# Kernel optimization log

Measured on AMD Instinct MI355X. Metric: run time of the kernel, lower is better.

## Reference

```python
import jax, jax.numpy as jnp
import numpy as np

B, D, U = 4096, 256, 512


def setup_inputs() -> dict:
    key = jax.random.key(0)
    k = jax.random.split(key, 7)
    return {
        "x": jax.random.normal(k[0], (B, D), jnp.float32),
        "t": jax.random.uniform(k[1], (B, 1), jnp.float32),           # elapsed-time input
        "h0": jax.random.normal(k[2], (B, U), jnp.float32),
        "c0": jax.random.normal(k[3], (B, U), jnp.float32),
        "kernel": jax.random.normal(k[4], (D, 5 * U), jnp.float32) / np.sqrt(D).astype(np.float32),
        "recurrent_kernel": jax.random.normal(k[5], (U, 3 * U), jnp.float32) / np.sqrt(U).astype(np.float32),
        "kernel_time": jax.random.normal(k[6], (1, 3 * U), jnp.float32) * 0.1,
    }


def reference(x, t, h0, c0, kernel, recurrent_kernel, kernel_time):
    sig = jax.nn.sigmoid
    # Fused input projection: one GEMM instead of 5 (same math, kernel cols are
    # ordered [i, c, o, t1, t2] exactly as the original slices self.kernel).
    x_i, x_c, x_o, x_t1, x_t2 = jnp.split(x @ kernel, 5, axis=1)          # each (B, U)
    # Fused recurrent projection: cols ordered [i, c, o].
    r_i, r_c, r_o = jnp.split(h0 @ recurrent_kernel, 3, axis=1)           # each (B, U)
    # Time projections: cols ordered [t1, t2, o].
    kt1, kt2, kto = jnp.split(t @ kernel_time, 3, axis=1)                 # each (B, U)

    i = sig(x_i + r_i)
    t_1 = sig(x_t1 + sig(kt1))
    # tf.where(t_1 > -1e-5, -1e-5, t_1): sigmoid output is always > -1e-5,
    # so this clamps to the constant -1e-5; keep the where for faithfulness.
    NEG_EPS = jnp.float32(-1e-5)
    t_1_constraint = jnp.where(t_1 > NEG_EPS, jnp.full_like(t_1, NEG_EPS), t_1)
    t_2 = sig(x_t2 + sig(kt2))
    c_tilde = jnp.tanh(x_c + r_c)
    c_m_ = (1.0 - i * t_1) * c0 + i * c_tilde * t_1_constraint
    c_m = (1.0 - i) * c0 + i * c_tilde * t_2
    o = sig(x_o + r_o + kto)
    h = jnp.tanh(c_m_) * o
    # original returns (h, [h, c_m]); h appears twice, so return (h, c_m)
    return (h, c_m)
```

## Files before the change

kernel.cpp:

```cpp
#include <hip/hip_runtime.h>


typedef __attribute__((ext_vector_type(8))) short short8_t;
typedef __attribute__((ext_vector_type(4))) float f32x4_t;
typedef unsigned int u32;

#define B_N 4096
#define D_K 256
#define U_N 512

__device__ __forceinline__ unsigned short f2bf(float f) {
    unsigned int x = __float_as_uint(f);
    unsigned int r = x + 0x7fffu + ((x >> 16) & 1u);
    return (unsigned short)(r >> 16);
}

__device__ __forceinline__ float sigf(float z) {
    return 1.0f / (1.0f + __expf(-z));
}

__device__ __forceinline__ void gl16(const unsigned short* g, unsigned short* l) {
    __builtin_amdgcn_global_load_lds(
        (const __attribute__((address_space(1))) u32*)g,
        (__attribute__((address_space(3))) u32*)l, 16, 0, 0);
}

#define SWZ(r, kc) ((((r) * 8) + ((kc) ^ ((r) & 7))) * 8)

__global__ __launch_bounds__(256) void prep(
    const float* __restrict__ x, const float* __restrict__ h0,
    const float* __restrict__ kern, const float* __restrict__ rk,
    unsigned short* __restrict__ xs, unsigned short* __restrict__ hs,
    unsigned short* __restrict__ ksw, unsigned short* __restrict__ rsw)
{
    const int c = blockIdx.x * 256 + threadIdx.x;
    if (c < 131072) {
        const int t = c >> 10, q = c & 1023;
        const int row = q >> 3, kc = q & 7;
        const int rb = t >> 2, kb = t & 3;
        const float* s = x + (size_t)(rb * 128 + row) * D_K + kb * 64 + kc * 8;
        short8_t o;
#pragma unroll
        for (int j = 0; j < 8; ++j) o[j] = (short)f2bf(s[j]);
        *reinterpret_cast<short8_t*>(xs + (size_t)t * 8192 + SWZ(row, kc)) = o;
    } else if (c < 393216) {
        const int c2 = c - 131072;
        const int t = c2 >> 10, q = c2 & 1023;
        const int row = q >> 3, kc = q & 7;
        const int rb = t >> 3, kb = t & 7;
        const float* s = h0 + (size_t)(rb * 128 + row) * U_N + kb * 64 + kc * 8;
        short8_t o;
#pragma unroll
        for (int j = 0; j < 8; ++j) o[j] = (short)f2bf(s[j]);
        *reinterpret_cast<short8_t*>(hs + (size_t)t * 8192 + SWZ(row, kc)) = o;
    } else if (c < 475136) {
        const int c2 = c - 393216;
        const int t = c2 / 1280, q = c2 - t * 1280;
        const int kc = q / 160, r = q - kc * 160;
        const int nb = t >> 2, kb = t & 3;
        const int col = (r >> 5) * U_N + nb * 32 + (r & 31);
        short8_t o;
#pragma unroll
        for (int j = 0; j < 8; ++j)
            o[j] = (short)f2bf(kern[(size_t)(kb * 64 + kc * 8 + j) * 2560 + col]);
        *reinterpret_cast<short8_t*>(ksw + (size_t)t * 10240 + SWZ(r, kc)) = o;
    } else {
        const int c2 = c - 475136;
        const int t = c2 / 768, q = c2 - t * 768;
        const int kc = q / 96, r = q - kc * 96;
        const int nb = t >> 3, kb = t & 7;
        const int col = (r >> 5) * U_N + nb * 32 + (r & 31);
        short8_t o;
#pragma unroll
        for (int j = 0; j < 8; ++j)
            o[j] = (short)f2bf(rk[(size_t)(kb * 64 + kc * 8 + j) * 1536 + col]);
        *reinterpret_cast<short8_t*>(rsw + (size_t)t * 6144 + SWZ(r, kc)) = o;
    }
}

__global__ __launch_bounds__(256, 2) void tlstm_main(
    const unsigned short* __restrict__ xs,
    const unsigned short* __restrict__ hs,
    const unsigned short* __restrict__ ksw,
    const unsigned short* __restrict__ rsw,
    const float* __restrict__ tvec,
    const float* __restrict__ c0,
    const float* __restrict__ ktime,
    float* __restrict__ out)
{
    __shared__ __align__(16) unsigned short lds[2][18432];

    const int tid = threadIdx.x;
    const int wave = tid >> 6;
    const int lane = tid & 63;
    const int lr = lane & 15;
    const int lq = lane >> 4;
    const int nb = blockIdx.x;
    const int rb = blockIdx.y;

    f32x4_t acc[8][2][2];
#pragma unroll
    for (int m = 0; m < 8; ++m)
#pragma unroll
        for (int p = 0; p < 2; ++p)
#pragma unroll
            for (int n = 0; n < 2; ++n)
                acc[m][p][n] = (f32x4_t){0.f, 0.f, 0.f, 0.f};

    auto stage = [&](int s, int buf) {
        unsigned short* ab = &lds[buf][0];
        unsigned short* bb = &lds[buf][8192];
        if (s < 4) {
            const unsigned short* at = xs + (size_t)(rb * 4 + s) * 8192;
#pragma unroll
            for (int j = 0; j < 4; ++j)
                gl16(at + (j * 256 + tid) * 8, ab + (j * 256 + wave * 64) * 8);
            const unsigned short* bt = ksw + (size_t)(nb * 4 + s) * 10240;
#pragma unroll
            for (int j = 0; j < 5; ++j)
                gl16(bt + (j * 256 + tid) * 8, bb + (j * 256 + wave * 64) * 8);
        } else {
            const unsigned short* at = hs + (size_t)(rb * 8 + (s - 4)) * 8192;
#pragma unroll
            for (int j = 0; j < 4; ++j)
                gl16(at + (j * 256 + tid) * 8, ab + (j * 256 + wave * 64) * 8);
            const unsigned short* bt = rsw + (size_t)(nb * 8 + (s - 4)) * 6144;
#pragma unroll
            for (int j = 0; j < 3; ++j)
                gl16(bt + (j * 256 + tid) * 8, bb + (j * 256 + wave * 64) * 8);
        }
    };

    auto compute1 = [&](int buf) {
        const unsigned short* ab = &lds[buf][0];
        const unsigned short* bb = &lds[buf][8192];
#pragma unroll
        for (int ks = 0; ks < 2; ++ks) {
            const int kc = ks * 4 + lq;
            const int r0 = wave * 32 + lr;
            short8_t a0 = *reinterpret_cast<const short8_t*>(ab + SWZ(r0, kc));
            short8_t a1 = *reinterpret_cast<const short8_t*>(ab + SWZ(r0 + 16, kc));
#pragma unroll
            for (int m = 0; m < 5; ++m)
#pragma unroll
                for (int n = 0; n < 2; ++n) {
                    const int r = m * 32 + n * 16 + lr;
                    short8_t b = *reinterpret_cast<const short8_t*>(bb + SWZ(r, kc));
                    acc[m][0][n] = __builtin_amdgcn_mfma_f32_16x16x32_bf16(a0, b, acc[m][0][n], 0, 0, 0);
                    acc[m][1][n] = __builtin_amdgcn_mfma_f32_16x16x32_bf16(a1, b, acc[m][1][n], 0, 0, 0);
                }
        }
    };

    auto compute2 = [&](int buf) {
        const unsigned short* ab = &lds[buf][0];
        const unsigned short* bb = &lds[buf][8192];
#pragma unroll
        for (int ks = 0; ks < 2; ++ks) {
            const int kc = ks * 4 + lq;
            const int r0 = wave * 32 + lr;
            short8_t a0 = *reinterpret_cast<const short8_t*>(ab + SWZ(r0, kc));
            short8_t a1 = *reinterpret_cast<const short8_t*>(ab + SWZ(r0 + 16, kc));
#pragma unroll
            for (int m = 0; m < 3; ++m)
#pragma unroll
                for (int n = 0; n < 2; ++n) {
                    const int r = m * 32 + n * 16 + lr;
                    short8_t b = *reinterpret_cast<const short8_t*>(bb + SWZ(r, kc));
                    acc[5 + m][0][n] = __builtin_amdgcn_mfma_f32_16x16x32_bf16(a0, b, acc[5 + m][0][n], 0, 0, 0);
                    acc[5 + m][1][n] = __builtin_amdgcn_mfma_f32_16x16x32_bf16(a1, b, acc[5 + m][1][n], 0, 0, 0);
                }
        }
    };

    int cur = 0;
    stage(0, 0);
    __syncthreads();
#pragma unroll 1
    for (int s = 0; s < 12; ++s) {
        if (s < 11) stage(s + 1, cur ^ 1);
        if (s < 4) compute1(cur); else compute2(cur);
        __syncthreads();
        cur ^= 1;
    }

    const float NEG_EPS = -1e-5f;
#pragma unroll
    for (int n = 0; n < 2; ++n) {
        const int u = nb * 32 + n * 16 + lr;
        const float kt1 = ktime[u];
        const float kt2 = ktime[U_N + u];
        const float kto = ktime[2 * U_N + u];
#pragma unroll
        for (int p = 0; p < 2; ++p)
#pragma unroll
            for (int i2 = 0; i2 < 4; ++i2) {
                const int b = rb * 128 + wave * 32 + p * 16 + lq * 4 + i2;
                const float tb = tvec[b];
                const float c0v = c0[(size_t)b * U_N + u];
                const float x_i  = acc[0][p][n][i2];
                const float x_c  = acc[1][p][n][i2];
                const float x_o  = acc[2][p][n][i2];
                const float x_t1 = acc[3][p][n][i2];
                const float x_t2 = acc[4][p][n][i2];
                const float r_i  = acc[5][p][n][i2];
                const float r_c  = acc[6][p][n][i2];
                const float r_o  = acc[7][p][n][i2];

                const float ig  = sigf(x_i + r_i);
                const float t1v = sigf(x_t1 + sigf(tb * kt1));
                const float t1c = (t1v > NEG_EPS) ? NEG_EPS : t1v;
                const float t2v = sigf(x_t2 + sigf(tb * kt2));
                const float ct  = tanhf(x_c + r_c);
                const float cm_ = (1.f - ig * t1v) * c0v + ig * ct * t1c;
                const float cm  = (1.f - ig) * c0v + ig * ct * t2v;
                const float og  = sigf(x_o + r_o + tb * kto);

                out[(size_t)b * U_N + u] = tanhf(cm_) * og;
                out[(size_t)B_N * U_N + (size_t)b * U_N + u] = cm;
            }
    }
}

extern "C" void kernel_launch(void* const* d_in, const int* in_sizes, int n_in,
                              void* d_out, int out_size, void* d_ws, size_t ws_size,
                              hipStream_t stream) {
    const float* x     = (const float*)d_in[0];
    const float* t     = (const float*)d_in[1];
    const float* h0    = (const float*)d_in[2];
    const float* c0    = (const float*)d_in[3];
    const float* kern  = (const float*)d_in[4];
    const float* rk    = (const float*)d_in[5];
    const float* ktime = (const float*)d_in[6];
    float* out = (float*)d_out;

    unsigned short* xs  = (unsigned short*)d_ws;
    unsigned short* hs  = (unsigned short*)((char*)d_ws + 2097152);
    unsigned short* ksw = (unsigned short*)((char*)d_ws + 6291456);
    unsigned short* rsw = (unsigned short*)((char*)d_ws + 7602176);

    prep<<<2240, 256, 0, stream>>>(x, h0, kern, rk, xs, hs, ksw, rsw);
    tlstm_main<<<dim3(16, 32), 256, 0, stream>>>(
        xs, hs, ksw, rsw, t, c0, ktime, out);
}
```

Before: 34.48 us.

## Retile waves to 2x2 grid and use exp-based fast tanh

Changes the wave layout from four waves each owning 32 rows by all gate columns to a 2x2 arrangement, with each wave owning 64 rows and 16 columns per gate. Each wave now loads 4 A fragments and one B fragment per gate and k-step instead of 2 A and 2 B. This cuts B-fragment LDS reads, which dominate because of the many gate tiles. It also replaces tanhf with an __expf-based formula in the epilogue to shorten transcendental cost, trading some accuracy and overflow behavior for extreme inputs.

```diff
diff --git a/kernel.cpp b/kernel.cpp
--- a/kernel.cpp
+++ b/kernel.cpp
@@ -17,6 +17,10 @@
 
 __device__ __forceinline__ float sigf(float z) {
     return 1.0f / (1.0f + __expf(-z));
+}
+
+__device__ __forceinline__ float tanhfast(float z) {
+    return 1.0f - 2.0f / (1.0f + __expf(2.0f * z));
 }
 
 __device__ __forceinline__ void gl16(const unsigned short* g, unsigned short* l) {
@@ -95,17 +99,17 @@
     const int lane = tid & 63;
     const int lr = lane & 15;
     const int lq = lane >> 4;
+    const int wm = wave >> 1;
+    const int wn = wave & 1;
     const int nb = blockIdx.x;
     const int rb = blockIdx.y;
 
-    f32x4_t acc[8][2][2];
+    f32x4_t acc[8][4];
 #pragma unroll
     for (int m = 0; m < 8; ++m)
 #pragma unroll
-        for (int p = 0; p < 2; ++p)
-#pragma unroll
-            for (int n = 0; n < 2; ++n)
-                acc[m][p][n] = (f32x4_t){0.f, 0.f, 0.f, 0.f};
+        for (int p = 0; p < 4; ++p)
+            acc[m][p] = (f32x4_t){0.f, 0.f, 0.f, 0.f};
 
     auto stage = [&](int s, int buf) {
         unsigned short* ab = &lds[buf][0];
@@ -137,18 +141,18 @@
 #pragma unroll
         for (int ks = 0; ks < 2; ++ks) {
             const int kc = ks * 4 + lq;
-            const int r0 = wave * 32 + lr;
-            short8_t a0 = *reinterpret_cast<const short8_t*>(ab + SWZ(r0, kc));
-            short8_t a1 = *reinterpret_cast<const short8_t*>(ab + SWZ(r0 + 16, kc));
-#pragma unroll
-            for (int m = 0; m < 5; ++m)
-#pragma unroll
-                for (int n = 0; n < 2; ++n) {
-                    const int r = m * 32 + n * 16 + lr;
-                    short8_t b = *reinterpret_cast<const short8_t*>(bb + SWZ(r, kc));
-                    acc[m][0][n] = __builtin_amdgcn_mfma_f32_16x16x32_bf16(a0, b, acc[m][0][n], 0, 0, 0);
-                    acc[m][1][n] = __builtin_amdgcn_mfma_f32_16x16x32_bf16(a1, b, acc[m][1][n], 0, 0, 0);
-                }
+            short8_t a[4];
+#pragma unroll
+            for (int p = 0; p < 4; ++p)
+                a[p] = *reinterpret_cast<const short8_t*>(ab + SWZ(wm * 64 + p * 16 + lr, kc));
+#pragma unroll
+            for (int m = 0; m < 5; ++m) {
+                const int r = m * 32 + wn * 16 + lr;
+                short8_t b = *reinterpret_cast<const short8_t*>(bb + SWZ(r, kc));
+#pragma unroll
+                for (int p = 0; p < 4; ++p)
+                    acc[m][p] = __builtin_amdgcn_mfma_f32_16x16x32_bf16(a[p], b, acc[m][p], 0, 0, 0);
+            }
         }
     };
 
@@ -158,18 +162,18 @@
 #pragma unroll
         for (int ks = 0; ks < 2; ++ks) {
             const int kc = ks * 4 + lq;
-            const int r0 = wave * 32 + lr;
-            short8_t a0 = *reinterpret_cast<const short8_t*>(ab + SWZ(r0, kc));
-            short8_t a1 = *reinterpret_cast<const short8_t*>(ab + SWZ(r0 + 16, kc));
-#pragma unroll
-            for (int m = 0; m < 3; ++m)
-#pragma unroll
-                for (int n = 0; n < 2; ++n) {
-                    const int r = m * 32 + n * 16 + lr;
-                    short8_t b = *reinterpret_cast<const short8_t*>(bb + SWZ(r, kc));
-                    acc[5 + m][0][n] = __builtin_amdgcn_mfma_f32_16x16x32_bf16(a0, b, acc[5 + m][0][n], 0, 0, 0);
-                    acc[5 + m][1][n] = __builtin_amdgcn_mfma_f32_16x16x32_bf16(a1, b, acc[5 + m][1][n], 0, 0, 0);
-                }
+            short8_t a[4];
+#pragma unroll
+            for (int p = 0; p < 4; ++p)
+                a[p] = *reinterpret_cast<const short8_t*>(ab + SWZ(wm * 64 + p * 16 + lr, kc));
+#pragma unroll
+            for (int m = 0; m < 3; ++m) {
+                const int r = m * 32 + wn * 16 + lr;
+                short8_t b = *reinterpret_cast<const short8_t*>(bb + SWZ(r, kc));
+#pragma unroll
+                for (int p = 0; p < 4; ++p)
+                    acc[5 + m][p] = __builtin_amdgcn_mfma_f32_16x16x32_bf16(a[p], b, acc[5 + m][p], 0, 0, 0);
+            }
         }
     };
 
@@ -185,41 +189,39 @@
     }
 
     const float NEG_EPS = -1e-5f;
-#pragma unroll
-    for (int n = 0; n < 2; ++n) {
-        const int u = nb * 32 + n * 16 + lr;
-        const float kt1 = ktime[u];
-        const float kt2 = ktime[U_N + u];
-        const float kto = ktime[2 * U_N + u];
-#pragma unroll
-        for (int p = 0; p < 2; ++p)
-#pragma unroll
-            for (int i2 = 0; i2 < 4; ++i2) {
-                const int b = rb * 128 + wave * 32 + p * 16 + lq * 4 + i2;
-                const float tb = tvec[b];
-                const float c0v = c0[(size_t)b * U_N + u];
-                const float x_i  = acc[0][p][n][i2];
-                const float x_c  = acc[1][p][n][i2];
-                const float x_o  = acc[2][p][n][i2];
-                const float x_t1 = acc[3][p][n][i2];
-                const float x_t2 = acc[4][p][n][i2];
-                const float r_i  = acc[5][p][n][i2];
-                const float r_c  = acc[6][p][n][i2];
-                const float r_o  = acc[7][p][n][i2];
-
-                const float ig  = sigf(x_i + r_i);
-                const float t1v = sigf(x_t1 + sigf(tb * kt1));
-                const float t1c = (t1v > NEG_EPS) ? NEG_EPS : t1v;
-                const float t2v = sigf(x_t2 + sigf(tb * kt2));
-                const float ct  = tanhf(x_c + r_c);
-                const float cm_ = (1.f - ig * t1v) * c0v + ig * ct * t1c;
-                const float cm  = (1.f - ig) * c0v + ig * ct * t2v;
-                const float og  = sigf(x_o + r_o + tb * kto);
-
-                out[(size_t)b * U_N + u] = tanhf(cm_) * og;
-                out[(size_t)B_N * U_N + (size_t)b * U_N + u] = cm;
-            }
-    }
+    const int u = nb * 32 + wn * 16 + lr;
+    const float kt1 = ktime[u];
+    const float kt2 = ktime[U_N + u];
+    const float kto = ktime[2 * U_N + u];
+#pragma unroll
+    for (int p = 0; p < 4; ++p)
+#pragma unroll
+        for (int i2 = 0; i2 < 4; ++i2) {
+            const int b = rb * 128 + wm * 64 + p * 16 + lq * 4 + i2;
+            const float tb = tvec[b];
+            const float c0v = c0[(size_t)b * U_N + u];
+            const float x_i  = acc[0][p][i2];
+            const float x_c  = acc[1][p][i2];
+            const float x_o  = acc[2][p][i2];
+            const float x_t1 = acc[3][p][i2];
+            const float x_t2 = acc[4][p][i2];
+            const float r_i  = acc[5][p][i2];
+            const float r_c  = acc[6][p][i2];
+            const float r_o  = acc[7][p][i2];
+
+            const float ig  = sigf(x_i + r_i);
+            const float t1v = sigf(x_t1 + sigf(tb * kt1));
+            const float t1c = (t1v > NEG_EPS) ? NEG_EPS : t1v;
+            const float t2v = sigf(x_t2 + sigf(tb * kt2));
+            const float ct  = tanhfast(x_c + r_c);
+            const float cm_ = (1.f - ig * t1v) * c0v + ig * ct * t1c;
+            const float cm  = (1.f - ig) * c0v + ig * ct * t2v;
+            const float og  = sigf(x_o + r_o + tb * kto);
+
+            out[(size_t)b * U_N + u] = tanhfast(cm_) * og;
+            out[(size_t)B_N * U_N + (size_t)b * U_N + u] = cm;
+        }
+
 }
 
 extern "C" void kernel_launch(void* const* d_in, const int* in_sizes, int n_in,
```

Result: faster. 33.19 us (-3.7%).
